# Kernel tuning notes

Hardware: AMD Instinct MI355X
Metric: run time of the kernel (lower is better)

Reference implementation:

```python
import jax, jax.numpy as jnp
import numpy as np

N, S, Q, P = 20000, 400, 20, 3


def setup_inputs() -> dict:
    key = jax.random.key(0)
    k1, k2, k3, k4 = jax.random.split(key, 4)
    # Learned parameters (post-projection state: non-negative, ~L2-normalized)
    heads_param = jax.random.uniform(k1, (S, Q, P), dtype=jnp.float32)
    heads_param = heads_param / jnp.linalg.norm(heads_param, axis=-1, keepdims=True)
    head_ratios_param = jax.random.uniform(k2, (S,), dtype=jnp.float32)
    head_ratios_param = head_ratios_param / jnp.linalg.norm(head_ratios_param)
    # Forward inputs
    batch_pauli_tensor = jax.random.uniform(k3, (N, Q, P), dtype=jnp.float32)
    batch_coeff = jax.random.normal(k4, (N,), dtype=jnp.float32)
    return {
        "heads_param": heads_param,
        "head_ratios_param": head_ratios_param,
        "batch_pauli_tensor": batch_pauli_tensor,
        "batch_coeff": batch_coeff,
    }


def reference(heads_param, head_ratios_param, batch_pauli_tensor, batch_coeff):
    p_exp = 2  # module-level constant `p`
    heads = heads_param ** p_exp              # [s,q,p]
    head_ratios = head_ratios_param ** p_exp  # [s]
    # coverage per (word, head, qubit): dot over Pauli axis
    shadow_coverage = jnp.einsum('nqp,sqp->nsq', batch_pauli_tensor, heads)  # [n,s,q]
    coverage = jnp.prod(shadow_coverage, axis=-1)                            # [n,s]
    coverage = jnp.einsum('s,ns->n', head_ratios, coverage)                  # [n]
    loss_val = jnp.sum((batch_coeff ** 2) / coverage)
    return (loss_val, head_ratios, heads)
```

## Files before the change

### kernel.cpp

```cpp
#include <hip/hip_runtime.h>

#define NN 20000
#define SS 400
#define QP 60
#define NPAIRS 10000
#define JPB 64
#define NBLK ((NPAIRS + JPB - 1)/JPB)
#define JPAD (NBLK*JPB)
#define NP2 (JPAD*2)
#define GSPLIT 5
#define SB (SS/GSPLIT)
#define WAVES 8
#define BLK_B (WAVES*64)
#define SW (SB/WAVES)
#define NC 5
#define PTF4 (JPB*30)
#define PF4TOT (NN*QP/4)

#define WS_H    0
#define WS_PT   (SS*QP)
#define WS_COV  (WS_PT + NBLK*PTF4*4)
#define CBLK    ((NP2 + 255)/256)

typedef float v2f __attribute__((ext_vector_type(2)));

__device__ __forceinline__ v2f lo4(float4 f) { v2f r; r.x = f.x; r.y = f.y; return r; }
__device__ __forceinline__ v2f hi4(float4 f) { v2f r; r.x = f.z; r.y = f.w; return r; }

__global__ __launch_bounds__(512) void prep_kernel(
        const float* __restrict__ heads_param,
        const float* __restrict__ ratios_param,
        const float* __restrict__ pauli,
        float* __restrict__ out, float* __restrict__ ws) {
    __shared__ float ldsR[JPB*2*QP];

    const int tid = threadIdx.x;
    const int bx  = blockIdx.x;

    {
        const float4* src = reinterpret_cast<const float4*>(pauli) + (size_t)bx * PTF4;
        float4* dst = reinterpret_cast<float4*>(ldsR);
        #pragma unroll
        for (int it = 0; it < 4; ++it) {
            int i = tid + it*512;
            if (i < PTF4) {
                int gi = bx*PTF4 + i;
                dst[i] = (gi < PF4TOT) ? src[i] : make_float4(0.f,0.f,0.f,0.f);
            }
        }
    }
    __syncthreads();

    {
        float4* pt = reinterpret_cast<float4*>(ws + WS_PT) + (size_t)bx * PTF4;
        #pragma unroll
        for (int it = 0; it < 4; ++it) {
            int i = tid + it*512;
            if (i < PTF4) {
                int k = i >> 6, l = i & 63;
                float4 v;
                v.x = ldsR[(2*l  )*QP + 2*k    ];
                v.y = ldsR[(2*l+1)*QP + 2*k    ];
                v.z = ldsR[(2*l  )*QP + 2*k + 1];
                v.w = ldsR[(2*l+1)*QP + 2*k + 1];
                pt[i] = v;
            }
        }
    }

    const int gi = bx*512 + tid;
    if (gi < SS*QP) {
        int s = gi / QP;
        int k = gi - s*QP;
        float h = heads_param[gi];
        float h2 = h * h;
        out[1 + SS + gi] = h2;
        float rr = ratios_param[s];
        float v = (k < 3) ? h2 * (rr*rr) : h2;
        int g  = s / SB, sl = s - g*SB;
        int c  = k / 12, kk = k - c*12;
        ws[WS_H + (((size_t)g*NC + c)*SB + sl)*12 + kk] = v;
    }
    if (gi < SS) {
        float rr = ratios_param[gi];
        out[1 + gi] = rr * rr;
    }
    if (gi == 0) out[0] = 0.f;
}

#define S_STEP(A, SI)                                                   \
    do {                                                                \
        const float4* hf = reinterpret_cast<const float4*>(hc + (SI)*12); \
        float4 f0 = hf[0], f1 = hf[1], f2 = hf[2];                      \
        v2f d0 = pq0*f0.x + pq1*f0.y  + pq2*f0.z;                       \
        v2f d1 = pq3*f0.w + pq4*f1.x  + pq5*f1.y;                       \
        v2f d2 = pq6*f1.z + pq7*f1.w  + pq8*f2.x;                       \
        v2f d3 = pq9*f2.y + pq10*f2.z + pq11*f2.w;                      \
        A *= (d0*d1)*(d2*d3);                                           \
    } while (0)

__global__ __launch_bounds__(BLK_B) void main_kernel(
        const float* __restrict__ hws,
        const float4* __restrict__ pt,
        float* __restrict__ cov) {
    __shared__ float4 ldsP[PTF4];
    __shared__ v2f    ldsC[WAVES][64];

    const int tid  = threadIdx.x;
    const int wave = __builtin_amdgcn_readfirstlane(tid >> 6);
    const int lane = tid & 63;
    const int g    = blockIdx.y;
    const int bx   = blockIdx.x;

    {
        const float4* src = pt + (size_t)bx * PTF4;
        for (int i = tid; i < PTF4; i += BLK_B) ldsP[i] = src[i];
    }
    __syncthreads();

    v2f one; one.x = 1.f; one.y = 1.f;
    v2f a0=one,a1=one,a2=one,a3=one,a4=one,a5=one,a6=one,a7=one,a8=one,a9=one;

    #pragma unroll 1
    for (int c = 0; c < NC; ++c) {
        const float* hc = hws + (((size_t)g*NC + c)*SB + wave*SW)*12;
        float4 q0 = ldsP[(c*6+0)*64+lane], q1 = ldsP[(c*6+1)*64+lane];
        float4 q2 = ldsP[(c*6+2)*64+lane], q3 = ldsP[(c*6+3)*64+lane];
        float4 q4 = ldsP[(c*6+4)*64+lane], q5 = ldsP[(c*6+5)*64+lane];
        v2f pq0 = lo4(q0), pq1  = hi4(q0), pq2  = lo4(q1), pq3  = hi4(q1);
        v2f pq4 = lo4(q2), pq5  = hi4(q2), pq6  = lo4(q3), pq7  = hi4(q3);
        v2f pq8 = lo4(q4), pq9  = hi4(q4), pq10 = lo4(q5), pq11 = hi4(q5);
        S_STEP(a0, 0); S_STEP(a1, 1); S_STEP(a2, 2); S_STEP(a3, 3); S_STEP(a4, 4);
        S_STEP(a5, 5); S_STEP(a6, 6); S_STEP(a7, 7); S_STEP(a8, 8); S_STEP(a9, 9);
    }

    v2f cv = (((a0+a1)+(a2+a3)) + ((a4+a5)+(a6+a7))) + (a8+a9);
    ldsC[wave][lane] = cv;
    __syncthreads();

    if (wave == 0) {
        v2f t = ldsC[0][lane];
        #pragma unroll
        for (int w = 1; w < WAVES; ++w) t += ldsC[w][lane];
        const int j = bx * JPB + lane;
        *reinterpret_cast<v2f*>(cov + (size_t)g * NP2 + 2*j) = t;
    }
}

__global__ void combine_kernel(const float* __restrict__ ws,
                               const float* __restrict__ coeff,
                               float* __restrict__ out) {
    __shared__ float red[4];
    const int tid = threadIdx.x;
    const int n = blockIdx.x * 256 + tid;
    float term = 0.f;
    if (n < NN) {
        float cov = 0.f;
        #pragma unroll
        for (int g = 0; g < GSPLIT; ++g) cov += ws[WS_COV + (size_t)g * NP2 + n];
        float c = coeff[n];
        term = (c * c) / cov;
    }
    #pragma unroll
    for (int off = 32; off; off >>= 1) term += __shfl_down(term, off);
    if ((tid & 63) == 0) red[tid >> 6] = term;
    __syncthreads();
    if (tid == 0) atomicAdd(out, red[0] + red[1] + red[2] + red[3]);
}

extern "C" void kernel_launch(void* const* d_in, const int* in_sizes, int n_in,
                              void* d_out, int out_size, void* d_ws, size_t ws_size,
                              hipStream_t stream) {
    const float* heads_param  = (const float*)d_in[0];
    const float* ratios_param = (const float*)d_in[1];
    const float* pauli        = (const float*)d_in[2];
    const float* coeff        = (const float*)d_in[3];
    float* out = (float*)d_out;
    float* ws  = (float*)d_ws;

    prep_kernel<<<NBLK, 512, 0, stream>>>(heads_param, ratios_param, pauli, out, ws);
    main_kernel<<<dim3(NBLK, GSPLIT), BLK_B, 0, stream>>>(
        ws + WS_H, (const float4*)(ws + WS_PT), ws + WS_COV);
    combine_kernel<<<CBLK, 256, 0, stream>>>(ws, coeff, out);
}
```

Before: 32.63 us.

## Fuse combine into main kernel via atomics and drop Pauli transpose pass

The prep kernel no longer transposes the Pauli tensor into workspace. The main kernel loads raw rows of it into LDS and computes each word's dot products with scalar FMAs instead of packed two-wide vectors. The separate combine kernel is removed: each head-group block atomically adds its partial coverage, and the last block per column group (found with an atomic counter) computes the coeff²/coverage terms and adds them to the loss. This saves one kernel launch and one workspace round-trip. The costs are possible loss of packed-FMA throughput, strided LDS reads with bank conflicts, and atomic traffic.

```diff
diff --git a/kernel.cpp b/kernel.cpp
--- a/kernel.cpp
+++ b/kernel.cpp
@@ -6,69 +6,26 @@
 #define NPAIRS 10000
 #define JPB 64
 #define NBLK ((NPAIRS + JPB - 1)/JPB)
-#define JPAD (NBLK*JPB)
-#define NP2 (JPAD*2)
+#define NP2 (NBLK*JPB*2)
 #define GSPLIT 5
 #define SB (SS/GSPLIT)
 #define WAVES 8
 #define BLK_B (WAVES*64)
 #define SW (SB/WAVES)
 #define NC 5
-#define PTF4 (JPB*30)
+#define RPB (JPB*2)
+#define RF4 (RPB*(QP/4))
 #define PF4TOT (NN*QP/4)
 
 #define WS_H    0
-#define WS_PT   (SS*QP)
-#define WS_COV  (WS_PT + NBLK*PTF4*4)
-#define CBLK    ((NP2 + 255)/256)
+#define WS_CS   (SS*QP)
+#define WS_CNT  (WS_CS + NP2)
 
-typedef float v2f __attribute__((ext_vector_type(2)));
-
-__device__ __forceinline__ v2f lo4(float4 f) { v2f r; r.x = f.x; r.y = f.y; return r; }
-__device__ __forceinline__ v2f hi4(float4 f) { v2f r; r.x = f.z; r.y = f.w; return r; }
-
-__global__ __launch_bounds__(512) void prep_kernel(
+__global__ __launch_bounds__(256) void prep_kernel(
         const float* __restrict__ heads_param,
         const float* __restrict__ ratios_param,
-        const float* __restrict__ pauli,
         float* __restrict__ out, float* __restrict__ ws) {
-    __shared__ float ldsR[JPB*2*QP];
-
-    const int tid = threadIdx.x;
-    const int bx  = blockIdx.x;
-
-    {
-        const float4* src = reinterpret_cast<const float4*>(pauli) + (size_t)bx * PTF4;
-        float4* dst = reinterpret_cast<float4*>(ldsR);
-        #pragma unroll
-        for (int it = 0; it < 4; ++it) {
-            int i = tid + it*512;
-            if (i < PTF4) {
-                int gi = bx*PTF4 + i;
-                dst[i] = (gi < PF4TOT) ? src[i] : make_float4(0.f,0.f,0.f,0.f);
-            }
-        }
-    }
-    __syncthreads();
-
-    {
-        float4* pt = reinterpret_cast<float4*>(ws + WS_PT) + (size_t)bx * PTF4;
-        #pragma unroll
-        for (int it = 0; it < 4; ++it) {
-            int i = tid + it*512;
-            if (i < PTF4) {
-                int k = i >> 6, l = i & 63;
-                float4 v;
-                v.x = ldsR[(2*l  )*QP + 2*k    ];
-                v.y = ldsR[(2*l+1)*QP + 2*k    ];
-                v.z = ldsR[(2*l  )*QP + 2*k + 1];
-                v.w = ldsR[(2*l+1)*QP + 2*k + 1];
-                pt[i] = v;
-            }
-        }
-    }
-
-    const int gi = bx*512 + tid;
+    const int gi = blockIdx.x * 256 + threadIdx.x;
     if (gi < SS*QP) {
         int s = gi / QP;
         int k = gi - s*QP;
@@ -85,26 +42,36 @@
         float rr = ratios_param[gi];
         out[1 + gi] = rr * rr;
     }
+    if (gi < NP2) ws[WS_CS + gi] = 0.f;
+    if (gi < NBLK) reinterpret_cast<int*>(ws + WS_CNT)[gi] = 0;
     if (gi == 0) out[0] = 0.f;
 }
 
-#define S_STEP(A, SI)                                                   \
+#define S_STEP(AX, AY, SI)                                              \
     do {                                                                \
         const float4* hf = reinterpret_cast<const float4*>(hc + (SI)*12); \
         float4 f0 = hf[0], f1 = hf[1], f2 = hf[2];                      \
-        v2f d0 = pq0*f0.x + pq1*f0.y  + pq2*f0.z;                       \
-        v2f d1 = pq3*f0.w + pq4*f1.x  + pq5*f1.y;                       \
-        v2f d2 = pq6*f1.z + pq7*f1.w  + pq8*f2.x;                       \
-        v2f d3 = pq9*f2.y + pq10*f2.z + pq11*f2.w;                      \
-        A *= (d0*d1)*(d2*d3);                                           \
+        float dA0 = fa0.x*f0.x + fa0.y*f0.y + fa0.z*f0.z;               \
+        float dA1 = fa0.w*f0.w + fa1.x*f1.x + fa1.y*f1.y;               \
+        float dA2 = fa1.z*f1.z + fa1.w*f1.w + fa2.x*f2.x;               \
+        float dA3 = fa2.y*f2.y + fa2.z*f2.z + fa2.w*f2.w;               \
+        float dB0 = fb0.x*f0.x + fb0.y*f0.y + fb0.z*f0.z;               \
+        float dB1 = fb0.w*f0.w + fb1.x*f1.x + fb1.y*f1.y;               \
+        float dB2 = fb1.z*f1.z + fb1.w*f1.w + fb2.x*f2.x;               \
+        float dB3 = fb2.y*f2.y + fb2.z*f2.z + fb2.w*f2.w;               \
+        AX *= (dA0*dA1)*(dA2*dA3);                                      \
+        AY *= (dB0*dB1)*(dB2*dB3);                                      \
     } while (0)
 
 __global__ __launch_bounds__(BLK_B) void main_kernel(
         const float* __restrict__ hws,
-        const float4* __restrict__ pt,
-        float* __restrict__ cov) {
-    __shared__ float4 ldsP[PTF4];
-    __shared__ v2f    ldsC[WAVES][64];
+        const float* __restrict__ pauli,
+        const float* __restrict__ coeff,
+        float* covsum,
+        int*   cnt,
+        float* out) {
+    __shared__ float  ldsR[RPB*QP];
+    __shared__ float2 ldsC[WAVES][64];
 
     const int tid  = threadIdx.x;
     const int wave = __builtin_amdgcn_readfirstlane(tid >> 6);
@@ -113,59 +80,63 @@
     const int bx   = blockIdx.x;
 
     {
-        const float4* src = pt + (size_t)bx * PTF4;
-        for (int i = tid; i < PTF4; i += BLK_B) ldsP[i] = src[i];
+        const float4* src = reinterpret_cast<const float4*>(pauli) + (size_t)bx * RF4;
+        float4* dst = reinterpret_cast<float4*>(ldsR);
+        const int lim = PF4TOT - bx * RF4;
+        for (int i = tid; i < RF4; i += BLK_B)
+            dst[i] = (i < lim) ? src[i] : make_float4(0.f, 0.f, 0.f, 0.f);
     }
     __syncthreads();
 
-    v2f one; one.x = 1.f; one.y = 1.f;
-    v2f a0=one,a1=one,a2=one,a3=one,a4=one,a5=one,a6=one,a7=one,a8=one,a9=one;
+    const float4* rowA = reinterpret_cast<const float4*>(ldsR + (2*lane  )*QP);
+    const float4* rowB = reinterpret_cast<const float4*>(ldsR + (2*lane+1)*QP);
+
+    float aX0=1.f,aX1=1.f,aX2=1.f,aX3=1.f,aX4=1.f,aX5=1.f,aX6=1.f,aX7=1.f,aX8=1.f,aX9=1.f;
+    float aY0=1.f,aY1=1.f,aY2=1.f,aY3=1.f,aY4=1.f,aY5=1.f,aY6=1.f,aY7=1.f,aY8=1.f,aY9=1.f;
 
     #pragma unroll 1
     for (int c = 0; c < NC; ++c) {
+        float4 fa0 = rowA[c*3+0], fa1 = rowA[c*3+1], fa2 = rowA[c*3+2];
+        float4 fb0 = rowB[c*3+0], fb1 = rowB[c*3+1], fb2 = rowB[c*3+2];
         const float* hc = hws + (((size_t)g*NC + c)*SB + wave*SW)*12;
-        float4 q0 = ldsP[(c*6+0)*64+lane], q1 = ldsP[(c*6+1)*64+lane];
-        float4 q2 = ldsP[(c*6+2)*64+lane], q3 = ldsP[(c*6+3)*64+lane];
-        float4 q4 = ldsP[(c*6+4)*64+lane], q5 = ldsP[(c*6+5)*64+lane];
-        v2f pq0 = lo4(q0), pq1  = hi4(q0), pq2  = lo4(q1), pq3  = hi4(q1);
-        v2f pq4 = lo4(q2), pq5  = hi4(q2), pq6  = lo4(q3), pq7  = hi4(q3);
-        v2f pq8 = lo4(q4), pq9  = hi4(q4), pq10 = lo4(q5), pq11 = hi4(q5);
-        S_STEP(a0, 0); S_STEP(a1, 1); S_STEP(a2, 2); S_STEP(a3, 3); S_STEP(a4, 4);
-        S_STEP(a5, 5); S_STEP(a6, 6); S_STEP(a7, 7); S_STEP(a8, 8); S_STEP(a9, 9);
+        S_STEP(aX0,aY0,0); S_STEP(aX1,aY1,1); S_STEP(aX2,aY2,2);
+        S_STEP(aX3,aY3,3); S_STEP(aX4,aY4,4); S_STEP(aX5,aY5,5);
+        S_STEP(aX6,aY6,6); S_STEP(aX7,aY7,7); S_STEP(aX8,aY8,8);
+        S_STEP(aX9,aY9,9);
     }
 
-    v2f cv = (((a0+a1)+(a2+a3)) + ((a4+a5)+(a6+a7))) + (a8+a9);
+    float2 cv;
+    cv.x = (((aX0+aX1)+(aX2+aX3)) + ((aX4+aX5)+(aX6+aX7))) + (aX8+aX9);
+    cv.y = (((aY0+aY1)+(aY2+aY3)) + ((aY4+aY5)+(aY6+aY7))) + (aY8+aY9);
     ldsC[wave][lane] = cv;
     __syncthreads();
 
     if (wave == 0) {
-        v2f t = ldsC[0][lane];
+        float2 t = ldsC[0][lane];
         #pragma unroll
-        for (int w = 1; w < WAVES; ++w) t += ldsC[w][lane];
-        const int j = bx * JPB + lane;
-        *reinterpret_cast<v2f*>(cov + (size_t)g * NP2 + 2*j) = t;
+        for (int w = 1; w < WAVES; ++w) {
+            float2 u = ldsC[w][lane];
+            t.x += u.x; t.y += u.y;
+        }
+        const int j  = bx * JPB + lane;
+        const int n0 = 2 * j;
+        atomicAdd(&covsum[n0],     t.x);
+        atomicAdd(&covsum[n0 + 1], t.y);
+        asm volatile("s_waitcnt vmcnt(0)" ::: "memory");
+        int old = 0;
+        if (lane == 0) old = atomicAdd(cnt + bx, 1);
+        old = __shfl(old, 0);
+        if (old == GSPLIT - 1) {
+            float cs0 = __hip_atomic_load(&covsum[n0],     __ATOMIC_RELAXED, __HIP_MEMORY_SCOPE_AGENT);
+            float cs1 = __hip_atomic_load(&covsum[n0 + 1], __ATOMIC_RELAXED, __HIP_MEMORY_SCOPE_AGENT);
+            float term = 0.f;
+            if (n0 < NN)     { float c0 = coeff[n0];     term += (c0*c0) / cs0; }
+            if (n0 + 1 < NN) { float c1 = coeff[n0 + 1]; term += (c1*c1) / cs1; }
+            #pragma unroll
+            for (int off = 32; off; off >>= 1) term += __shfl_down(term, off);
+            if (lane == 0) atomicAdd(out, term);
+        }
     }
-}
-
-__global__ void combine_kernel(const float* __restrict__ ws,
-                               const float* __restrict__ coeff,
-                               float* __restrict__ out) {
-    __shared__ float red[4];
-    const int tid = threadIdx.x;
-    const int n = blockIdx.x * 256 + tid;
-    float term = 0.f;
-    if (n < NN) {
-        float cov = 0.f;
-        #pragma unroll
-        for (int g = 0; g < GSPLIT; ++g) cov += ws[WS_COV + (size_t)g * NP2 + n];
-        float c = coeff[n];
-        term = (c * c) / cov;
-    }
-    #pragma unroll
-    for (int off = 32; off; off >>= 1) term += __shfl_down(term, off);
-    if ((tid & 63) == 0) red[tid >> 6] = term;
-    __syncthreads();
-    if (tid == 0) atomicAdd(out, red[0] + red[1] + red[2] + red[3]);
 }
 
 extern "C" void kernel_launch(void* const* d_in, const int* in_sizes, int n_in,
@@ -178,8 +149,7 @@
     float* out = (float*)d_out;
     float* ws  = (float*)d_ws;
 
-    prep_kernel<<<NBLK, 512, 0, stream>>>(heads_param, ratios_param, pauli, out, ws);
+    prep_kernel<<<(SS*QP + 255)/256, 256, 0, stream>>>(heads_param, ratios_param, out, ws);
     main_kernel<<<dim3(NBLK, GSPLIT), BLK_B, 0, stream>>>(
-        ws + WS_H, (const float4*)(ws + WS_PT), ws + WS_COV);
-    combine_kernel<<<CBLK, 256, 0, stream>>>(ws, coeff, out);
+        ws + WS_H, pauli, coeff, ws + WS_CS, (int*)(ws + WS_CNT), out);
 }
```

Result: slower. 37.59 us (+15.2%).
